# Kernel tuning notes

Hardware: AMD Instinct MI355X
Metric: run time of the kernel (lower is better)

Reference implementation:

```python
import jax, jax.numpy as jnp
import numpy as np

C = 3               # BSARec cutoff hyperparameter
CUTOFF = max(1, C // 2 + 1)  # number of low-frequency bins kept = 2
LN_EPS = 1e-5       # torch LayerNorm default


def setup_inputs() -> dict:
    key = jax.random.key(0)
    k1, k2 = jax.random.split(key)
    B, S, H = 64, 2048, 256
    x = jax.random.normal(k1, (B, S, H), dtype=jnp.float32)
    sqrt_beta = jax.random.normal(k2, (1, 1, H), dtype=jnp.float32)
    ln_weight = jnp.ones((H,), dtype=jnp.float32)
    ln_bias = jnp.zeros((H,), dtype=jnp.float32)
    return {"x": x, "sqrt_beta": sqrt_beta, "ln_weight": ln_weight, "ln_bias": ln_bias}


def _layer_norm(h, weight, bias):
    mean = jnp.mean(h, axis=-1, keepdims=True)
    var = jnp.mean(jnp.square(h - mean), axis=-1, keepdims=True)
    return (h - mean) * jax.lax.rsqrt(var + LN_EPS) * weight + bias


def reference(x, sqrt_beta, ln_weight, ln_bias):
    B, S, H = x.shape
    # orthonormal rFFT along the sequence axis
    x_fft = jnp.fft.rfft(x, axis=1, norm="ortho")          # [B, S//2+1, H] complex
    freq_bins = x_fft.shape[1]
    cutoff = min(freq_bins, CUTOFF)
    # zero all bins >= cutoff (low-pass)
    bin_idx = jnp.arange(freq_bins)[None, :, None]
    low_fft = jnp.where(bin_idx < cutoff, x_fft, 0.0 + 0.0j)
    low_pass = jnp.fft.irfft(low_fft, n=S, axis=1, norm="ortho")  # [B, S, H]
    high_pass = x - low_pass
    seq = low_pass + jnp.square(sqrt_beta) * high_pass
    # dropout is identity at eval time
    return _layer_norm(seq + x, ln_weight, ln_bias)
```

## Files before the change

### kernel.cpp

```cpp
#include <hip/hip_runtime.h>

#define B_DIM 64
#define S_LEN 2048
#define H_DIM 256
#define TWO_PI 6.283185307179586f

__global__ __launch_bounds__(256) void k_partial(const float* __restrict__ x,
                                                 float* __restrict__ partials,
                                                 int rows_per_split) {
    const int b = blockIdx.x;
    const int split = blockIdx.y;
    const int tid = threadIdx.x;
    const int lane = tid & 63;
    const int wave = tid >> 6;
    const int h0 = lane * 4;

    float s0[4] = {0.f, 0.f, 0.f, 0.f};
    float c1[4] = {0.f, 0.f, 0.f, 0.f};
    float s1[4] = {0.f, 0.f, 0.f, 0.f};

    const int t_begin = split * rows_per_split;
    const int t_end = t_begin + rows_per_split;
    const float wfreq = TWO_PI / (float)S_LEN;

    for (int t = t_begin + wave; t < t_end; t += 4) {
        const float4 v = *reinterpret_cast<const float4*>(
            x + ((size_t)b * S_LEN + t) * H_DIM + h0);
        float sn, cs;
        __sincosf(wfreq * (float)t, &sn, &cs);
        s0[0] += v.x;      s0[1] += v.y;      s0[2] += v.z;      s0[3] += v.w;
        c1[0] += v.x * cs; c1[1] += v.y * cs; c1[2] += v.z * cs; c1[3] += v.w * cs;
        s1[0] += v.x * sn; s1[1] += v.y * sn; s1[2] += v.z * sn; s1[3] += v.w * sn;
    }

    __shared__ float red[4][3 * H_DIM];
#pragma unroll
    for (int j = 0; j < 4; ++j) {
        red[wave][0 * H_DIM + h0 + j] = s0[j];
        red[wave][1 * H_DIM + h0 + j] = c1[j];
        red[wave][2 * H_DIM + h0 + j] = s1[j];
    }
    __syncthreads();

#pragma unroll
    for (int k = 0; k < 3; ++k) {
        const int v = tid + k * 256;
        const float acc = red[0][v] + red[1][v] + red[2][v] + red[3][v];
        partials[((size_t)(split * B_DIM + b)) * (3 * H_DIM) + v] = acc;
    }
}

__global__ __launch_bounds__(256) void k_reduce(const float* __restrict__ partials,
                                                float* __restrict__ sums,
                                                int nsplit) {
    const int j = blockIdx.x * 256 + threadIdx.x;
    float acc = 0.f;
    for (int s = 0; s < nsplit; ++s)
        acc += partials[(size_t)s * (B_DIM * 3 * H_DIM) + j];
    sums[j] = acc;
}

#define ROWS_PER_BLOCK 16
__global__ __launch_bounds__(256) void k_final(const float* __restrict__ x,
                                               const float* __restrict__ sums,
                                               const float* __restrict__ sqrt_beta,
                                               const float* __restrict__ lnw,
                                               const float* __restrict__ lnb,
                                               float* __restrict__ out) {
    const int blocks_per_b = S_LEN / ROWS_PER_BLOCK;
    const int b = blockIdx.x / blocks_per_b;
    const int tchunk = blockIdx.x % blocks_per_b;
    const int tid = threadIdx.x;
    const int lane = tid & 63;
    const int wave = tid >> 6;

    __shared__ float sS0[H_DIM], sC1[H_DIM], sS1[H_DIM];
    __shared__ float sCA[H_DIM], sCB[H_DIM], sW[H_DIM], sBi[H_DIM];
    {
        const int h = tid;
        sS0[h] = sums[b * 768 + h];
        sC1[h] = sums[b * 768 + 256 + h];
        sS1[h] = sums[b * 768 + 512 + h];
        const float sb = sqrt_beta[h];
        const float b2 = sb * sb;
        sCA[h] = 1.f + b2;
        sCB[h] = 1.f - b2;
        sW[h] = lnw[h];
        sBi[h] = lnb[h];
    }
    __syncthreads();

    const float invS = 1.f / (float)S_LEN;
    const float wfreq = TWO_PI / (float)S_LEN;
    const int h0 = lane * 4;

#pragma unroll
    for (int r = 0; r < ROWS_PER_BLOCK / 4; ++r) {
        const int t = tchunk * ROWS_PER_BLOCK + wave * (ROWS_PER_BLOCK / 4) + r;
        float sn, cs;
        __sincosf(wfreq * (float)t, &sn, &cs);

        const size_t base = ((size_t)b * S_LEN + t) * H_DIM + h0;
        const float4 v = *reinterpret_cast<const float4*>(x + base);
        const float xf[4] = {v.x, v.y, v.z, v.w};

        float y[4];
        float sum = 0.f, sumsq = 0.f;
#pragma unroll
        for (int j = 0; j < 4; ++j) {
            const int h = h0 + j;
            const float lp = invS * (sS0[h] + 2.f * (sC1[h] * cs + sS1[h] * sn));
            const float yy = sCB[h] * lp + sCA[h] * xf[j];
            y[j] = yy;
            sum += yy;
            sumsq += yy * yy;
        }
#pragma unroll
        for (int m = 1; m < 64; m <<= 1) {
            sum += __shfl_xor(sum, m, 64);
            sumsq += __shfl_xor(sumsq, m, 64);
        }
        const float mean = sum * (1.f / (float)H_DIM);
        const float var = sumsq * (1.f / (float)H_DIM) - mean * mean;
        const float rstd = rsqrtf(var + 1e-5f);

        float4 o;
        o.x = (y[0] - mean) * rstd * sW[h0 + 0] + sBi[h0 + 0];
        o.y = (y[1] - mean) * rstd * sW[h0 + 1] + sBi[h0 + 1];
        o.z = (y[2] - mean) * rstd * sW[h0 + 2] + sBi[h0 + 2];
        o.w = (y[3] - mean) * rstd * sW[h0 + 3] + sBi[h0 + 3];
        *reinterpret_cast<float4*>(out + base) = o;
    }
}

extern "C" void kernel_launch(void* const* d_in, const int* in_sizes, int n_in,
                              void* d_out, int out_size, void* d_ws, size_t ws_size,
                              hipStream_t stream) {
    const float* x  = (const float*)d_in[0];
    const float* sb = (const float*)d_in[1];
    const float* w  = (const float*)d_in[2];
    const float* bi = (const float*)d_in[3];
    float* out = (float*)d_out;

    int nsplit = 16;
    while (nsplit > 1 &&
           ((size_t)(nsplit + 1) * B_DIM * 3 * H_DIM * sizeof(float)) > ws_size)
        nsplit >>= 1;
    float* partials = (float*)d_ws;
    float* sums = partials + (size_t)nsplit * B_DIM * 3 * H_DIM;

    k_partial<<<dim3(B_DIM, nsplit), 256, 0, stream>>>(x, partials, S_LEN / nsplit);
    k_reduce<<<(B_DIM * 3 * H_DIM) / 256, 256, 0, stream>>>(partials, sums, nsplit);
    k_final<<<B_DIM * (S_LEN / ROWS_PER_BLOCK), 256, 0, stream>>>(x, sums, sb, w, bi, out);
}
```

Baseline: 72.68 us.

## Vectorize partial and final kernels, use contiguous rows, nontemporal stores, more splits

The partial-sum kernel now gives each wave a contiguous block of rows and unrolls by two with vector accumulators, and the split count rises from 16 to 32 for more parallelism. The final kernel keeps per-column constants in registers instead of staging them through shared memory, drops the block barrier, processes 32 rows per block, and writes output with nontemporal stores to avoid cache pollution. The aim is to cut instruction overhead and improve the memory streaming of this bandwidth-bound op. The cost is more partials traffic in the reduce step and fewer blocks in the final kernel.

```diff
diff --git a/kernel.cpp b/kernel.cpp
--- a/kernel.cpp
+++ b/kernel.cpp
@@ -5,9 +5,11 @@
 #define H_DIM 256
 #define TWO_PI 6.283185307179586f
 
+typedef float f32x4 __attribute__((ext_vector_type(4)));
+
 __global__ __launch_bounds__(256) void k_partial(const float* __restrict__ x,
                                                  float* __restrict__ partials,
-                                                 int rows_per_split) {
+                                                 int rows_per_split, int nsplit_b) {
     const int b = blockIdx.x;
     const int split = blockIdx.y;
     const int tid = threadIdx.x;
@@ -15,30 +17,32 @@
     const int wave = tid >> 6;
     const int h0 = lane * 4;
 
-    float s0[4] = {0.f, 0.f, 0.f, 0.f};
-    float c1[4] = {0.f, 0.f, 0.f, 0.f};
-    float s1[4] = {0.f, 0.f, 0.f, 0.f};
-
-    const int t_begin = split * rows_per_split;
-    const int t_end = t_begin + rows_per_split;
+    const int rows_per_wave = rows_per_split >> 2;
+    const int t0 = split * rows_per_split + wave * rows_per_wave;
+    const float* px = x + ((size_t)b * S_LEN + t0) * H_DIM + h0;
     const float wfreq = TWO_PI / (float)S_LEN;
 
-    for (int t = t_begin + wave; t < t_end; t += 4) {
-        const float4 v = *reinterpret_cast<const float4*>(
-            x + ((size_t)b * S_LEN + t) * H_DIM + h0);
-        float sn, cs;
-        __sincosf(wfreq * (float)t, &sn, &cs);
-        s0[0] += v.x;      s0[1] += v.y;      s0[2] += v.z;      s0[3] += v.w;
-        c1[0] += v.x * cs; c1[1] += v.y * cs; c1[2] += v.z * cs; c1[3] += v.w * cs;
-        s1[0] += v.x * sn; s1[1] += v.y * sn; s1[2] += v.z * sn; s1[3] += v.w * sn;
+    f32x4 s0v = {0.f, 0.f, 0.f, 0.f};
+    f32x4 c1v = {0.f, 0.f, 0.f, 0.f};
+    f32x4 s1v = {0.f, 0.f, 0.f, 0.f};
+
+    for (int r = 0; r < rows_per_wave; r += 2) {
+        const f32x4 v0 = *reinterpret_cast<const f32x4*>(px + (size_t)r * H_DIM);
+        const f32x4 v1 = *reinterpret_cast<const f32x4*>(px + (size_t)(r + 1) * H_DIM);
+        float sn0, cs0, sn1, cs1;
+        __sincosf(wfreq * (float)(t0 + r), &sn0, &cs0);
+        __sincosf(wfreq * (float)(t0 + r + 1), &sn1, &cs1);
+        s0v += v0 + v1;
+        c1v += v0 * cs0 + v1 * cs1;
+        s1v += v0 * sn0 + v1 * sn1;
     }
 
     __shared__ float red[4][3 * H_DIM];
 #pragma unroll
     for (int j = 0; j < 4; ++j) {
-        red[wave][0 * H_DIM + h0 + j] = s0[j];
-        red[wave][1 * H_DIM + h0 + j] = c1[j];
-        red[wave][2 * H_DIM + h0 + j] = s1[j];
+        red[wave][0 * H_DIM + h0 + j] = s0v[j];
+        red[wave][1 * H_DIM + h0 + j] = c1v[j];
+        red[wave][2 * H_DIM + h0 + j] = s1v[j];
     }
     __syncthreads();
 
@@ -60,61 +64,48 @@
     sums[j] = acc;
 }
 
-#define ROWS_PER_BLOCK 16
+#define FROWS 32
 __global__ __launch_bounds__(256) void k_final(const float* __restrict__ x,
                                                const float* __restrict__ sums,
                                                const float* __restrict__ sqrt_beta,
                                                const float* __restrict__ lnw,
                                                const float* __restrict__ lnb,
                                                float* __restrict__ out) {
-    const int blocks_per_b = S_LEN / ROWS_PER_BLOCK;
+    const int blocks_per_b = S_LEN / FROWS;
     const int b = blockIdx.x / blocks_per_b;
     const int tchunk = blockIdx.x % blocks_per_b;
     const int tid = threadIdx.x;
     const int lane = tid & 63;
     const int wave = tid >> 6;
+    const int h0 = lane * 4;
 
-    __shared__ float sS0[H_DIM], sC1[H_DIM], sS1[H_DIM];
-    __shared__ float sCA[H_DIM], sCB[H_DIM], sW[H_DIM], sBi[H_DIM];
-    {
-        const int h = tid;
-        sS0[h] = sums[b * 768 + h];
-        sC1[h] = sums[b * 768 + 256 + h];
-        sS1[h] = sums[b * 768 + 512 + h];
-        const float sb = sqrt_beta[h];
-        const float b2 = sb * sb;
-        sCA[h] = 1.f + b2;
-        sCB[h] = 1.f - b2;
-        sW[h] = lnw[h];
-        sBi[h] = lnb[h];
-    }
-    __syncthreads();
+    const f32x4 S0 = *reinterpret_cast<const f32x4*>(sums + b * 768 + h0);
+    const f32x4 C1 = *reinterpret_cast<const f32x4*>(sums + b * 768 + 256 + h0);
+    const f32x4 S1 = *reinterpret_cast<const f32x4*>(sums + b * 768 + 512 + h0);
+    const f32x4 sb = *reinterpret_cast<const f32x4*>(sqrt_beta + h0);
+    const f32x4 Wv = *reinterpret_cast<const f32x4*>(lnw + h0);
+    const f32x4 Bv = *reinterpret_cast<const f32x4*>(lnb + h0);
+    const f32x4 b2 = sb * sb;
+    const f32x4 CA = b2 + 1.f;
+    const f32x4 CB = 1.f - b2;
 
     const float invS = 1.f / (float)S_LEN;
     const float wfreq = TWO_PI / (float)S_LEN;
-    const int h0 = lane * 4;
+    const int tbase = tchunk * FROWS + wave * (FROWS / 4);
+    const float* __restrict__ pxr = x + ((size_t)b * S_LEN + tbase) * H_DIM + h0;
+    float* __restrict__ por = out + ((size_t)b * S_LEN + tbase) * H_DIM + h0;
 
 #pragma unroll
-    for (int r = 0; r < ROWS_PER_BLOCK / 4; ++r) {
-        const int t = tchunk * ROWS_PER_BLOCK + wave * (ROWS_PER_BLOCK / 4) + r;
+    for (int r = 0; r < FROWS / 4; ++r) {
         float sn, cs;
-        __sincosf(wfreq * (float)t, &sn, &cs);
+        __sincosf(wfreq * (float)(tbase + r), &sn, &cs);
 
-        const size_t base = ((size_t)b * S_LEN + t) * H_DIM + h0;
-        const float4 v = *reinterpret_cast<const float4*>(x + base);
-        const float xf[4] = {v.x, v.y, v.z, v.w};
+        const f32x4 v = *reinterpret_cast<const f32x4*>(pxr + (size_t)r * H_DIM);
+        const f32x4 lp = (S0 + (C1 * cs + S1 * sn) * 2.f) * invS;
+        const f32x4 y = CB * lp + CA * v;
 
-        float y[4];
-        float sum = 0.f, sumsq = 0.f;
-#pragma unroll
-        for (int j = 0; j < 4; ++j) {
-            const int h = h0 + j;
-            const float lp = invS * (sS0[h] + 2.f * (sC1[h] * cs + sS1[h] * sn));
-            const float yy = sCB[h] * lp + sCA[h] * xf[j];
-            y[j] = yy;
-            sum += yy;
-            sumsq += yy * yy;
-        }
+        float sum = y.x + y.y + y.z + y.w;
+        float sumsq = y.x * y.x + y.y * y.y + y.z * y.z + y.w * y.w;
 #pragma unroll
         for (int m = 1; m < 64; m <<= 1) {
             sum += __shfl_xor(sum, m, 64);
@@ -124,12 +115,8 @@
         const float var = sumsq * (1.f / (float)H_DIM) - mean * mean;
         const float rstd = rsqrtf(var + 1e-5f);
 
-        float4 o;
-        o.x = (y[0] - mean) * rstd * sW[h0 + 0] + sBi[h0 + 0];
-        o.y = (y[1] - mean) * rstd * sW[h0 + 1] + sBi[h0 + 1];
-        o.z = (y[2] - mean) * rstd * sW[h0 + 2] + sBi[h0 + 2];
-        o.w = (y[3] - mean) * rstd * sW[h0 + 3] + sBi[h0 + 3];
-        *reinterpret_cast<float4*>(out + base) = o;
+        f32x4 o = (y - mean) * rstd * Wv + Bv;
+        __builtin_nontemporal_store(o, reinterpret_cast<f32x4*>(por + (size_t)r * H_DIM));
     }
 }
 
@@ -142,14 +129,14 @@
     const float* bi = (const float*)d_in[3];
     float* out = (float*)d_out;
 
-    int nsplit = 16;
+    int nsplit = 32;
     while (nsplit > 1 &&
            ((size_t)(nsplit + 1) * B_DIM * 3 * H_DIM * sizeof(float)) > ws_size)
         nsplit >>= 1;
     float* partials = (float*)d_ws;
     float* sums = partials + (size_t)nsplit * B_DIM * 3 * H_DIM;
 
-    k_partial<<<dim3(B_DIM, nsplit), 256, 0, stream>>>(x, partials, S_LEN / nsplit);
+    k_partial<<<dim3(B_DIM, nsplit), 256, 0, stream>>>(x, partials, S_LEN / nsplit, nsplit);
     k_reduce<<<(B_DIM * 3 * H_DIM) / 256, 256, 0, stream>>>(partials, sums, nsplit);
-    k_final<<<B_DIM * (S_LEN / ROWS_PER_BLOCK), 256, 0, stream>>>(x, sums, sb, w, bi, out);
+    k_final<<<B_DIM * (S_LEN / FROWS), 256, 0, stream>>>(x, sums, sb, w, bi, out);
 }
```

Result: slower. 81.98 us (+12.8%).
